# Optimization experiments

Hardware: AMD Instinct MI355X
Metric: run time of the kernel (lower is better)

Reference implementation:

```python
import jax, jax.numpy as jnp
import numpy as np

B, N, D = 32, 64, 512


def setup_inputs() -> dict:
    key = jax.random.key(0)
    k1, k2, k3 = jax.random.split(key, 3)
    s_e = jax.random.normal(k1, (B, N, N, D), dtype=jnp.float32)
    adjacency_matrix = jax.random.randint(k2, (B, N, N), 0, 2).astype(jnp.float32)
    W = jax.random.normal(k3, (D, 1), dtype=jnp.float32) * (1.0 / np.sqrt(D))
    b = jnp.zeros((1,), dtype=jnp.float32)
    return {"s_e": s_e, "adjacency_matrix": adjacency_matrix, "W": W, "b": b}


def reference(s_e, adjacency_matrix, W, b):
    Bn, Nn, _, Dn = s_e.shape
    # zero out the sub<->obj self edges before masking
    adj = adjacency_matrix.at[:, 0, 1].set(0.0).at[:, 1, 0].set(0.0)
    # EDGESCORE: per-edge linear score D -> 1 over all N*N edges
    score = (jnp.einsum('bijd,do->bij', s_e, W) + b[0]) * adj  # [B,N,N]
    s_e_score = score[:, :2]                                   # [B,2,N]
    sub_max_score_id = jnp.argmax(s_e_score[:, 0], axis=-1)    # [B]
    obj_max_score_id = jnp.argmax(s_e_score[:, 1], axis=-1)    # [B]
    # torch's mask_sub/mask_obj writes are self-assignments (no-op)
    final_id = jnp.stack([sub_max_score_id, obj_max_score_id], axis=-1)  # [B,2]
    sub_pos = sub_max_score_id > 0
    obj_pos = obj_max_score_id > 0
    flag = jnp.where(sub_pos & obj_pos, 3.0,
           jnp.where(sub_pos, 1.0,
           jnp.where(obj_pos, 2.0, 0.0))).astype(jnp.float32)  # [B]
    return final_id, s_e_score, flag
```

## Files before the change

### kernel.cpp

```cpp
#include <hip/hip_runtime.h>


#define BB 32
#define NN 64
#define DD 512

__global__ __launch_bounds__(1024) void subgraph_kernel(
    const float* __restrict__ s_e,
    const float* __restrict__ adj,
    const float* __restrict__ W,
    const float* __restrict__ bias,
    float* __restrict__ out)
{
    const int b    = blockIdx.x;
    const int tid  = threadIdx.x;
    const int wave = tid >> 6;
    const int lane = tid & 63;

    __shared__ float scores[2][NN];
    __shared__ int   ids[2];

    const float4 w0 = *reinterpret_cast<const float4*>(W + lane * 8);
    const float4 w1 = *reinterpret_cast<const float4*>(W + lane * 8 + 4);
    const float  b0 = bias[0];

    for (int p = wave; p < 2 * NN; p += 16) {
        const int i = p >> 6;
        const int j = p & 63;
        const float* base =
            s_e + (((size_t)b * NN + i) * NN + j) * DD + lane * 8;
        const float4 a0 = *reinterpret_cast<const float4*>(base);
        const float4 a1 = *reinterpret_cast<const float4*>(base + 4);
        float s = a0.x * w0.x + a0.y * w0.y + a0.z * w0.z + a0.w * w0.w
                + a1.x * w1.x + a1.y * w1.y + a1.z * w1.z + a1.w * w1.w;
        #pragma unroll
        for (int off = 32; off; off >>= 1)
            s += __shfl_xor(s, off, 64);
        if (lane == 0) {
            float a = adj[((size_t)b * NN + i) * NN + j];
            if ((i == 0 && j == 1) || (i == 1 && j == 0)) a = 0.0f;
            scores[i][j] = (s + b0) * a;
        }
    }
    __syncthreads();

    if (tid < 2) {
        const int i = tid;
        float best  = scores[i][0];
        int   bestj = 0;
        for (int j = 1; j < NN; ++j) {
            const float v = scores[i][j];
            if (v > best) { best = v; bestj = j; }
        }
        ids[i] = bestj;
        out[b * 2 + i] = (float)bestj;
    }
    __syncthreads();

    if (tid < 128) {
        out[BB * 2 + b * 128 + tid] = scores[tid >> 6][tid & 63];
    }
    if (tid == 0) {
        const bool sp = ids[0] > 0;
        const bool op = ids[1] > 0;
        const float flag = (sp && op) ? 3.0f : (sp ? 1.0f : (op ? 2.0f : 0.0f));
        out[BB * 2 + BB * 2 * NN + b] = flag;
    }
}

extern "C" void kernel_launch(void* const* d_in, const int* in_sizes, int n_in,
                              void* d_out, int out_size, void* d_ws, size_t ws_size,
                              hipStream_t stream) {
    const float* s_e  = (const float*)d_in[0];
    const float* adj  = (const float*)d_in[1];
    const float* W    = (const float*)d_in[2];
    const float* bias = (const float*)d_in[3];
    float* out = (float*)d_out;

    subgraph_kernel<<<BB, 1024, 0, stream>>>(s_e, adj, W, bias, out);
}
```

Measured before the change: 306.4 us.

## Split score rows across blocks, batch loads per wave, move flag to second kernel

Launches one block per (batch, row) pair instead of one per batch, doubling the number of blocks from 32 to 64 on a GPU with many CUs. Each wave now issues all four of its row loads up front before reducing, so more memory requests are in flight at once. Because the flag depends on both rows' argmax, a tiny second kernel computes it from the stored ids. That adds a second launch on the stream.

```diff
diff --git a/kernel.cpp b/kernel.cpp
--- a/kernel.cpp
+++ b/kernel.cpp
@@ -5,66 +5,83 @@
 #define NN 64
 #define DD 512
 
-__global__ __launch_bounds__(1024) void subgraph_kernel(
+__global__ __launch_bounds__(1024) void score_kernel(
     const float* __restrict__ s_e,
     const float* __restrict__ adj,
     const float* __restrict__ W,
     const float* __restrict__ bias,
     float* __restrict__ out)
 {
-    const int b    = blockIdx.x;
+    const int bi   = blockIdx.x;
+    const int b    = bi >> 1;
+    const int i    = bi & 1;
     const int tid  = threadIdx.x;
     const int wave = tid >> 6;
     const int lane = tid & 63;
 
-    __shared__ float scores[2][NN];
-    __shared__ int   ids[2];
+    __shared__ float scores[NN];
 
     const float4 w0 = *reinterpret_cast<const float4*>(W + lane * 8);
     const float4 w1 = *reinterpret_cast<const float4*>(W + lane * 8 + 4);
     const float  b0 = bias[0];
 
-    for (int p = wave; p < 2 * NN; p += 16) {
-        const int i = p >> 6;
-        const int j = p & 63;
-        const float* base =
-            s_e + (((size_t)b * NN + i) * NN + j) * DD + lane * 8;
-        const float4 a0 = *reinterpret_cast<const float4*>(base);
-        const float4 a1 = *reinterpret_cast<const float4*>(base + 4);
-        float s = a0.x * w0.x + a0.y * w0.y + a0.z * w0.z + a0.w * w0.w
-                + a1.x * w1.x + a1.y * w1.y + a1.z * w1.z + a1.w * w1.w;
+    const float* rowbase = s_e + (((size_t)b * NN + i) * NN) * DD + lane * 8;
+
+    float4 a[4][2];
+    #pragma unroll
+    for (int k = 0; k < 4; ++k) {
+        const int j = wave + 16 * k;
+        a[k][0] = *reinterpret_cast<const float4*>(rowbase + (size_t)j * DD);
+        a[k][1] = *reinterpret_cast<const float4*>(rowbase + (size_t)j * DD + 4);
+    }
+
+    float s[4];
+    #pragma unroll
+    for (int k = 0; k < 4; ++k) {
+        s[k] = a[k][0].x * w0.x + a[k][0].y * w0.y + a[k][0].z * w0.z + a[k][0].w * w0.w
+             + a[k][1].x * w1.x + a[k][1].y * w1.y + a[k][1].z * w1.z + a[k][1].w * w1.w;
+    }
+
+    #pragma unroll
+    for (int off = 32; off; off >>= 1) {
         #pragma unroll
-        for (int off = 32; off; off >>= 1)
-            s += __shfl_xor(s, off, 64);
-        if (lane == 0) {
-            float a = adj[((size_t)b * NN + i) * NN + j];
-            if ((i == 0 && j == 1) || (i == 1 && j == 0)) a = 0.0f;
-            scores[i][j] = (s + b0) * a;
+        for (int k = 0; k < 4; ++k)
+            s[k] += __shfl_xor(s[k], off, 64);
+    }
+
+    if (lane == 0) {
+        #pragma unroll
+        for (int k = 0; k < 4; ++k) {
+            const int j = wave + 16 * k;
+            float av = adj[((size_t)b * NN + i) * NN + j];
+            if ((i == 0 && j == 1) || (i == 1 && j == 0)) av = 0.0f;
+            scores[j] = (s[k] + b0) * av;
         }
     }
     __syncthreads();
 
-    if (tid < 2) {
-        const int i = tid;
-        float best  = scores[i][0];
+    if (tid < NN)
+        out[BB * 2 + (size_t)bi * NN + tid] = scores[tid];
+
+    if (tid == 0) {
+        float best  = scores[0];
         int   bestj = 0;
         for (int j = 1; j < NN; ++j) {
-            const float v = scores[i][j];
+            const float v = scores[j];
             if (v > best) { best = v; bestj = j; }
         }
-        ids[i] = bestj;
-        out[b * 2 + i] = (float)bestj;
+        out[bi] = (float)bestj;
     }
-    __syncthreads();
+}
 
-    if (tid < 128) {
-        out[BB * 2 + b * 128 + tid] = scores[tid >> 6][tid & 63];
-    }
-    if (tid == 0) {
-        const bool sp = ids[0] > 0;
-        const bool op = ids[1] > 0;
-        const float flag = (sp && op) ? 3.0f : (sp ? 1.0f : (op ? 2.0f : 0.0f));
-        out[BB * 2 + BB * 2 * NN + b] = flag;
+__global__ void flag_kernel(float* __restrict__ out)
+{
+    const int b = threadIdx.x;
+    if (b < BB) {
+        const bool sp = out[b * 2]     > 0.5f;
+        const bool op = out[b * 2 + 1] > 0.5f;
+        out[BB * 2 + BB * 2 * NN + b] =
+            (sp && op) ? 3.0f : (sp ? 1.0f : (op ? 2.0f : 0.0f));
     }
 }
 
@@ -77,5 +94,6 @@
     const float* bias = (const float*)d_in[3];
     float* out = (float*)d_out;
 
-    subgraph_kernel<<<BB, 1024, 0, stream>>>(s_e, adj, W, bias, out);
+    score_kernel<<<BB * 2, 1024, 0, stream>>>(s_e, adj, W, bias, out);
+    flag_kernel<<<1, 64, 0, stream>>>(out);
 }
```

Result: no change. 301.5 us (-1.6%).
